# Optimization experiments

Measured on AMD Instinct MI355X. Metric: run time of the kernel, lower is better.

Reference implementation:

```python
import jax, jax.numpy as jnp
import numpy as np

NB, D, ED, N, K, DTR = 4, 1024, 2048, 32, 4, 64
B, L = 1, 1024


def setup_inputs():
    key = jax.random.key(0)
    ks = jax.random.split(key, 10)
    g = lambda k, s, sc=0.02: jax.random.normal(k, s, dtype=jnp.float32) * sc
    A_log = jnp.log(jnp.broadcast_to(jnp.arange(1, N + 1, dtype=jnp.float32), (NB, ED, N))) + 0.0
    return {
        "x": g(ks[0], (B, L, D), 1.0),
        "Wi": g(ks[1], (D, D)),
        "bi": jnp.zeros((D,), jnp.float32),
        "ln_g": jnp.ones((NB, D), jnp.float32),
        "ln_b": jnp.zeros((NB, D), jnp.float32),
        "in_w": g(ks[2], (NB, 2 * ED, D)),
        "conv_w": g(ks[3], (NB, ED, 1, K), 0.2),
        "conv_b": jnp.zeros((NB, ED), jnp.float32),
        "xproj_w": g(ks[4], (NB, DTR + 2 * N, ED)),
        "dtproj_w": g(ks[5], (NB, ED, DTR), 0.1),
        "dtproj_b": jnp.full((NB, ED), -4.0, jnp.float32),
        "A_log": A_log,
        "Dp": jnp.ones((NB, ED), jnp.float32),
        "out_w": g(ks[6], (NB, D, ED)),
        "fn_g": jnp.ones((D,), jnp.float32),
        "fn_b": jnp.zeros((D,), jnp.float32),
        "sp_w": g(ks[7], (N, D)),
        "sp_b": jnp.zeros((N,), jnp.float32),
    }


def layernorm(x, g, b, eps=1e-5):
    m = jnp.mean(x, axis=-1, keepdims=True)
    v = jnp.mean(jnp.square(x - m), axis=-1, keepdims=True)
    return (x - m) * jax.lax.rsqrt(v + eps) * g + b


def mamba(u_in, in_w, conv_w, conv_b, xproj_w, dtproj_w, dtproj_b, A_log, Dp, out_w):
    # u_in: (B, L, D)
    xz = u_in @ in_w.T                       # (B, L, 2*ED)
    u, z = jnp.split(xz, 2, axis=-1)         # each (B, L, ED)
    # causal depthwise conv over time
    uc = jnp.swapaxes(u, 1, 2)               # (B, ED, L)
    uc = jax.lax.conv_general_dilated(uc, conv_w, (1,), [(K - 1, 0)], feature_group_count=ED)
    uc = uc + conv_b[None, :, None]
    u = jax.nn.silu(jnp.swapaxes(uc, 1, 2))  # (B, L, ED)
    x_dbl = u @ xproj_w.T                    # (B, L, DTR + 2N)
    dt, Bm, Cm = jnp.split(x_dbl, [DTR, DTR + N], axis=-1)
    delta = jax.nn.softplus(dt @ dtproj_w.T + dtproj_b)  # (B, L, ED)
    A = -jnp.exp(A_log)                                  # (ED, N)
    dA = jnp.exp(delta[..., None] * A)                   # (B, L, ED, N)
    dBu = (delta * u)[..., None] * Bm[:, :, None, :]     # (B, L, ED, N)

    def step(h, inp):
        dA_t, dBu_t, C_t = inp
        h = dA_t * h + dBu_t
        y = jnp.einsum('ben,bn->be', h, C_t)
        return h, y

    h0 = jnp.zeros((u.shape[0], ED, N), u.dtype)
    _, ys = jax.lax.scan(step, h0, (jnp.swapaxes(dA, 0, 1), jnp.swapaxes(dBu, 0, 1), jnp.swapaxes(Cm, 0, 1)))
    y = jnp.swapaxes(ys, 0, 1) + u * Dp      # (B, L, ED)
    y = y * jax.nn.silu(z)
    return y @ out_w.T                       # (B, L, D)


def reference(x, Wi, bi, ln_g, ln_b, in_w, conv_w, conv_b, xproj_w, dtproj_w, dtproj_b, A_log, Dp, out_w, fn_g, fn_b, sp_w, sp_b):
    h = x @ Wi.T + bi
    for i in range(NB):
        normed = layernorm(h, ln_g[i], ln_b[i])
        h = h + mamba(normed, in_w[i], conv_w[i], conv_b[i], xproj_w[i],
                      dtproj_w[i], dtproj_b[i], A_log[i], Dp[i], out_w[i])
    h = layernorm(h, fn_g, fn_b)
    state = jnp.mean(h, axis=1) @ sp_w.T + sp_b   # (B, N)
    return h, state
```

## Files before the change

kernel.cpp:

```cpp
#include <hip/hip_runtime.h>
#include <math.h>

#define D_    1024
#define ED_   2048
#define NST   32
#define KCONV 4
#define DTR_  64
#define L_    1024
#define NB_   4
#define NCH   8
#define CHUNK (L_ / NCH)
#define ZSPL  4
#define XPZ   16

typedef __bf16 bf16_8 __attribute__((ext_vector_type(8)));
typedef __bf16 bf16_4 __attribute__((ext_vector_type(4)));
typedef float  f32x4  __attribute__((ext_vector_type(4)));

__device__ __forceinline__ float softplus_f(float x) {
  return x > 20.f ? x : log1pf(expf(x));
}
__device__ __forceinline__ float silu_f(float x) {
  return x / (1.f + expf(-x));
}

__device__ __forceinline__ int xcd_swz(int lin, int nwg) {
  const int q = nwg >> 3;
  return (lin & 7) * q + (lin >> 3);
}

__global__ __launch_bounds__(256) void f2bf4_k(
    const float* __restrict__ i0, __bf16* __restrict__ o0, int n0,
    const float* __restrict__ i1, __bf16* __restrict__ o1, int n1,
    const float* __restrict__ i2, __bf16* __restrict__ o2, int n2,
    const float* __restrict__ i3, __bf16* __restrict__ o3, int n3)
{
  int gid = blockIdx.x * 256 + threadIdx.x;
  const int u0 = n0 >> 3, u1 = n1 >> 3, u2 = n2 >> 3, u3 = n3 >> 3;
  const float* in; __bf16* out;
  if (gid < u0) { in = i0; out = o0; }
  else if ((gid -= u0) < u1) { in = i1; out = o1; }
  else if ((gid -= u1) < u2) { in = i2; out = o2; }
  else if ((gid -= u2) < u3) { in = i3; out = o3; }
  else return;
  const int i = gid * 8;
  const float4 a = *reinterpret_cast<const float4*>(in + i);
  const float4 b = *reinterpret_cast<const float4*>(in + i + 4);
  bf16_8 v;
  v[0]=(__bf16)a.x; v[1]=(__bf16)a.y; v[2]=(__bf16)a.z; v[3]=(__bf16)a.w;
  v[4]=(__bf16)b.x; v[5]=(__bf16)b.y; v[6]=(__bf16)b.z; v[7]=(__bf16)b.w;
  *reinterpret_cast<bf16_8*>(out + i) = v;
}

__global__ __launch_bounds__(256) void gemm_mfma(
    const __bf16* __restrict__ A, int lda,
    const __bf16* __restrict__ W, int ldw,
    const float* __restrict__ bias, float* __restrict__ C, int ldc,
    int K, int flags)
{
  __shared__ __bf16 As[128 * 64];
  __shared__ __bf16 Ws[128 * 64];
  const int tid  = threadIdx.x;
  const int lane = tid & 63;
  const int w    = tid >> 6;
  const int wr   = w >> 1, wc = w & 1;
  const int nwg  = gridDim.x * gridDim.y;
  const int swz  = xcd_swz(blockIdx.y * gridDim.x + blockIdx.x, nwg);
  const int bx   = swz % gridDim.x, by = swz / gridDim.x;
  const int row0 = by * 128, col0 = bx * 128;

  f32x4 acc[4][4] = {};

  for (int k0 = 0; k0 < K; k0 += 64) {
    #pragma unroll
    for (int j = 0; j < 4; ++j) {
      const int inst = w * 4 + j;
      const int row  = inst * 8 + (lane >> 3);
      const int lu   = (lane & 7) ^ (row & 7);
      __builtin_amdgcn_global_load_lds(
          (const __attribute__((address_space(1))) void*)(A + (size_t)(row0 + row) * lda + k0 + lu * 8),
          (__attribute__((address_space(3))) void*)(&As[inst * 512]), 16, 0, 0);
      __builtin_amdgcn_global_load_lds(
          (const __attribute__((address_space(1))) void*)(W + (size_t)(col0 + row) * ldw + k0 + lu * 8),
          (__attribute__((address_space(3))) void*)(&Ws[inst * 512]), 16, 0, 0);
    }
    __syncthreads();
    const int r16 = lane & 15;
    const int uq  = lane >> 4;
    #pragma unroll
    for (int ks = 0; ks < 2; ++ks) {
      bf16_8 af[4], bfr[4];
      #pragma unroll
      for (int m = 0; m < 4; ++m) {
        const int row = wr * 64 + m * 16 + r16;
        const int pu  = (ks * 4 + uq) ^ (row & 7);
        af[m] = *reinterpret_cast<const bf16_8*>(&As[row * 64 + pu * 8]);
      }
      #pragma unroll
      for (int n = 0; n < 4; ++n) {
        const int row = wc * 64 + n * 16 + r16;
        const int pu  = (ks * 4 + uq) ^ (row & 7);
        bfr[n] = *reinterpret_cast<const bf16_8*>(&Ws[row * 64 + pu * 8]);
      }
      #pragma unroll
      for (int m = 0; m < 4; ++m)
        #pragma unroll
        for (int n = 0; n < 4; ++n)
          acc[m][n] = __builtin_amdgcn_mfma_f32_16x16x32_bf16(af[m], bfr[n], acc[m][n], 0, 0, 0);
    }
    __syncthreads();
  }

  const int crow = (lane >> 4) * 4;
  const int ccol = lane & 15;
  #pragma unroll
  for (int m = 0; m < 4; ++m)
    #pragma unroll
    for (int n = 0; n < 4; ++n) {
      const int col = col0 + wc * 64 + n * 16 + ccol;
      const float bv = (flags & 4) ? bias[col] : 0.f;
      #pragma unroll
      for (int r = 0; r < 4; ++r) {
        const int row = row0 + wr * 64 + m * 16 + crow + r;
        float* cp = C + (size_t)row * ldc + col;
        float v = acc[m][n][r] + bv;
        if (flags & 2) v = softplus_f(v);
        if (flags & 1) v += *cp;
        *cp = v;
      }
    }
}

__global__ __launch_bounds__(256) void gemm_mfma_sk(
    const __bf16* __restrict__ A, const __bf16* __restrict__ W,
    float* __restrict__ partials, int M, int N, int K, int Kc)
{
  __shared__ __bf16 As[128 * 64];
  __shared__ __bf16 Ws[128 * 64];
  const int tid  = threadIdx.x;
  const int lane = tid & 63;
  const int w    = tid >> 6;
  const int wr   = w >> 1, wc = w & 1;
  const int nwg  = gridDim.x * gridDim.y * gridDim.z;
  const int lin  = (blockIdx.z * gridDim.y + blockIdx.y) * gridDim.x + blockIdx.x;
  const int swz  = xcd_swz(lin, nwg);
  const int bx   = swz % gridDim.x;
  const int tmp  = swz / gridDim.x;
  const int by   = tmp % gridDim.y, bz = tmp / gridDim.y;
  const int row0 = by * 128, col0 = bx * 128;
  const int kbase = bz * Kc;

  f32x4 acc[4][4] = {};

  for (int k0 = kbase; k0 < kbase + Kc; k0 += 64) {
    #pragma unroll
    for (int j = 0; j < 4; ++j) {
      const int inst = w * 4 + j;
      const int row  = inst * 8 + (lane >> 3);
      const int lu   = (lane & 7) ^ (row & 7);
      __builtin_amdgcn_global_load_lds(
          (const __attribute__((address_space(1))) void*)(A + (size_t)(row0 + row) * K + k0 + lu * 8),
          (__attribute__((address_space(3))) void*)(&As[inst * 512]), 16, 0, 0);
      __builtin_amdgcn_global_load_lds(
          (const __attribute__((address_space(1))) void*)(W + (size_t)(col0 + row) * K + k0 + lu * 8),
          (__attribute__((address_space(3))) void*)(&Ws[inst * 512]), 16, 0, 0);
    }
    __syncthreads();
    const int r16 = lane & 15;
    const int uq  = lane >> 4;
    #pragma unroll
    for (int ks = 0; ks < 2; ++ks) {
      bf16_8 af[4], bfr[4];
      #pragma unroll
      for (int m = 0; m < 4; ++m) {
        const int row = wr * 64 + m * 16 + r16;
        const int pu  = (ks * 4 + uq) ^ (row & 7);
        af[m] = *reinterpret_cast<const bf16_8*>(&As[row * 64 + pu * 8]);
      }
      #pragma unroll
      for (int n = 0; n < 4; ++n) {
        const int row = wc * 64 + n * 16 + r16;
        const int pu  = (ks * 4 + uq) ^ (row & 7);
        bfr[n] = *reinterpret_cast<const bf16_8*>(&Ws[row * 64 + pu * 8]);
      }
      #pragma unroll
      for (int m = 0; m < 4; ++m)
        #pragma unroll
        for (int n = 0; n < 4; ++n)
          acc[m][n] = __builtin_amdgcn_mfma_f32_16x16x32_bf16(af[m], bfr[n], acc[m][n], 0, 0, 0);
    }
    __syncthreads();
  }

  float* base = partials + (size_t)bz * M * N;
  const int crow = (lane >> 4) * 4;
  const int ccol = lane & 15;
  #pragma unroll
  for (int m = 0; m < 4; ++m)
    #pragma unroll
    for (int n = 0; n < 4; ++n) {
      const int col = col0 + wc * 64 + n * 16 + ccol;
      #pragma unroll
      for (int r = 0; r < 4; ++r) {
        const int row = row0 + wr * 64 + m * 16 + crow + r;
        base[(size_t)row * N + col] = acc[m][n][r];
      }
    }
}

__global__ __launch_bounds__(256) void mfma_sk_reduce(
    const float* __restrict__ partials, const float* __restrict__ bias,
    float* __restrict__ C, __bf16* __restrict__ Cbf,
    int elems, int ncols, int nz, int flags)
{
  const int i = (blockIdx.x * 256 + threadIdx.x) * 4;
  if (i >= elems) return;
  float4 s = *reinterpret_cast<const float4*>(partials + i);
  for (int z = 1; z < nz; ++z) {
    const float4 p = *reinterpret_cast<const float4*>(partials + (size_t)z * elems + i);
    s.x += p.x; s.y += p.y; s.z += p.z; s.w += p.w;
  }
  if (flags & 4) {
    const float4 bv = *reinterpret_cast<const float4*>(bias + (i % ncols));
    s.x += bv.x; s.y += bv.y; s.z += bv.z; s.w += bv.w;
  }
  if (flags & 1) {
    const float4 ov = *reinterpret_cast<const float4*>(C + i);
    s.x += ov.x; s.y += ov.y; s.z += ov.z; s.w += ov.w;
  }
  *reinterpret_cast<float4*>(C + i) = s;
  if (flags & 8) {
    bf16_4 b;
    b[0]=(__bf16)s.x; b[1]=(__bf16)s.y; b[2]=(__bf16)s.z; b[3]=(__bf16)s.w;
    *reinterpret_cast<bf16_4*>(Cbf + i) = b;
  }
}

__global__ __launch_bounds__(256) void layernorm_k(
    const float* __restrict__ x, const float* __restrict__ g,
    const float* __restrict__ b, float* __restrict__ out)
{
  __shared__ float red[8];
  const int row = blockIdx.x;
  const int tid = threadIdx.x;
  const float* xr = x + (size_t)row * D_;
  float4 v = *reinterpret_cast<const float4*>(xr + tid * 4);
  float s = v.x + v.y + v.z + v.w;
  #pragma unroll
  for (int off = 32; off; off >>= 1) s += __shfl_down(s, off, 64);
  if ((tid & 63) == 0) red[tid >> 6] = s;
  __syncthreads();
  const float m = (red[0] + red[1] + red[2] + red[3]) * (1.f / D_);
  float dx0 = v.x - m, dx1 = v.y - m, dx2 = v.z - m, dx3 = v.w - m;
  float ss = dx0*dx0 + dx1*dx1 + dx2*dx2 + dx3*dx3;
  #pragma unroll
  for (int off = 32; off; off >>= 1) ss += __shfl_down(ss, off, 64);
  if ((tid & 63) == 0) red[4 + (tid >> 6)] = ss;
  __syncthreads();
  const float var = (red[4] + red[5] + red[6] + red[7]) * (1.f / D_);
  const float rs = rsqrtf(var + 1e-5f);
  const int c = tid * 4;
  const float4 gv = *reinterpret_cast<const float4*>(g + c);
  const float4 bv = *reinterpret_cast<const float4*>(b + c);
  float4 o;
  o.x = dx0 * rs * gv.x + bv.x;
  o.y = dx1 * rs * gv.y + bv.y;
  o.z = dx2 * rs * gv.z + bv.z;
  o.w = dx3 * rs * gv.w + bv.w;
  *reinterpret_cast<float4*>(out + (size_t)row * D_ + c) = o;
}

__global__ __launch_bounds__(256) void layernorm_bf_k(
    const float* __restrict__ x, const float* __restrict__ g,
    const float* __restrict__ b, __bf16* __restrict__ out)
{
  __shared__ float red[8];
  const int row = blockIdx.x;
  const int tid = threadIdx.x;
  const float* xr = x + (size_t)row * D_;
  float4 v = *reinterpret_cast<const float4*>(xr + tid * 4);
  float s = v.x + v.y + v.z + v.w;
  #pragma unroll
  for (int off = 32; off; off >>= 1) s += __shfl_down(s, off, 64);
  if ((tid & 63) == 0) red[tid >> 6] = s;
  __syncthreads();
  const float m = (red[0] + red[1] + red[2] + red[3]) * (1.f / D_);
  float dx0 = v.x - m, dx1 = v.y - m, dx2 = v.z - m, dx3 = v.w - m;
  float ss = dx0*dx0 + dx1*dx1 + dx2*dx2 + dx3*dx3;
  #pragma unroll
  for (int off = 32; off; off >>= 1) ss += __shfl_down(ss, off, 64);
  if ((tid & 63) == 0) red[4 + (tid >> 6)] = ss;
  __syncthreads();
  const float var = (red[4] + red[5] + red[6] + red[7]) * (1.f / D_);
  const float rs = rsqrtf(var + 1e-5f);
  const int c = tid * 4;
  const float4 gv = *reinterpret_cast<const float4*>(g + c);
  const float4 bv = *reinterpret_cast<const float4*>(b + c);
  bf16_4 o;
  o[0] = (__bf16)(dx0 * rs * gv.x + bv.x);
  o[1] = (__bf16)(dx1 * rs * gv.y + bv.y);
  o[2] = (__bf16)(dx2 * rs * gv.z + bv.z);
  o[3] = (__bf16)(dx3 * rs * gv.w + bv.w);
  *reinterpret_cast<bf16_4*>(out + (size_t)row * D_ + c) = o;
}

__global__ __launch_bounds__(256) void conv_silu_k(
    const float* __restrict__ xz, const float* __restrict__ cw,
    const float* __restrict__ cb, float* __restrict__ u, __bf16* __restrict__ ub)
{
  const int e = blockIdx.x * 256 + threadIdx.x;
  const int t0 = blockIdx.y * 8;
  const float w0 = cw[e*4+0], w1 = cw[e*4+1], w2 = cw[e*4+2], w3 = cw[e*4+3];
  const float b = cb[e];
  float x0 = (t0 >= 3) ? xz[(size_t)(t0-3)*(2*ED_)+e] : 0.f;
  float x1 = (t0 >= 2) ? xz[(size_t)(t0-2)*(2*ED_)+e] : 0.f;
  float x2 = (t0 >= 1) ? xz[(size_t)(t0-1)*(2*ED_)+e] : 0.f;
  #pragma unroll
  for (int j = 0; j < 8; ++j) {
    const float x3 = xz[(size_t)(t0+j)*(2*ED_)+e];
    const float uv = silu_f(b + w0*x0 + w1*x1 + w2*x2 + w3*x3);
    u[(size_t)(t0+j)*ED_+e] = uv;
    ub[(size_t)(t0+j)*ED_+e] = (__bf16)uv;
    x0 = x1; x1 = x2; x2 = x3;
  }
}

__global__ __launch_bounds__(512) void scan_phase1(
    const float* __restrict__ delta, const float* __restrict__ u,
    const float* __restrict__ xdbl, const float* __restrict__ A_log,
    float* __restrict__ hend, float* __restrict__ Pend)
{
  __shared__ float dl[16][16], ul[16][16];
  __shared__ float bl[16][36];
  const int tid = threadIdx.x;
  const int n = tid & 31;
  const int c = tid >> 5;
  const int e0 = blockIdx.x * 16;
  const int e = e0 + c;
  const int ch = blockIdx.y;
  const float a = -expf(A_log[e * NST + n]);
  float h = 0.f, S = 0.f;
  const int t0 = ch * CHUNK;
  const int s_t = (tid & 255) >> 4, s_e = tid & 15;
  const int bidx = tid - 256;
  const int b_t = bidx >> 3, b_c = (bidx & 7) * 4;

  float rg_a = 0.f;
  float4 rg_b;
  if (tid < 256) {
    rg_a = delta[(size_t)(t0 + s_t) * ED_ + e0 + s_e];
  } else {
    rg_a = u[(size_t)(t0 + s_t) * ED_ + e0 + s_e];
    if (bidx < 128)
      rg_b = *reinterpret_cast<const float4*>(&xdbl[(size_t)(t0 + b_t) * 128 + 64 + b_c]);
  }

  for (int tb = 0; tb < CHUNK; tb += 16) {
    if (tid < 256) {
      dl[s_t][s_e] = rg_a;
    } else {
      ul[s_t][s_e] = rg_a;
      if (bidx < 128) *reinterpret_cast<float4*>(&bl[b_t][b_c]) = rg_b;
    }
    __syncthreads();
    if (tb + 16 < CHUNK) {
      const int t = t0 + tb + 16 + s_t;
      if (tid < 256) {
        rg_a = delta[(size_t)t * ED_ + e0 + s_e];
      } else {
        rg_a = u[(size_t)t * ED_ + e0 + s_e];
        if (bidx < 128)
          rg_b = *reinterpret_cast<const float4*>(&xdbl[(size_t)(t0 + tb + 16 + b_t) * 128 + 64 + b_c]);
      }
    }
    #pragma unroll
    for (int j = 0; j < 16; ++j) {
      const float sd = dl[j][c];
      const float uv = ul[j][c];
      const float Bv = bl[j][n];
      h = fmaf(__expf(sd * a), h, sd * uv * Bv);
      S += sd;
    }
    __syncthreads();
  }
  const int idx = ch * (ED_ * NST) + blockIdx.x * 512 + tid;
  hend[idx] = h;
  Pend[idx] = __expf(a * S);
}

__global__ __launch_bounds__(512) void scan_phase3(
    const float* __restrict__ delta, const float* __restrict__ u,
    const float* __restrict__ xdbl, const float* __restrict__ A_log,
    const float* __restrict__ hend, const float* __restrict__ Pend,
    const float* __restrict__ Dp,
    const float* __restrict__ xz, __bf16* __restrict__ y)
{
  __shared__ float p_lds[16][16][33];
  __shared__ float dl[16][16], ul[16][16], zl[16][16];
  __shared__ float bc[16][68];
  const int tid = threadIdx.x;
  const int n = tid & 31;
  const int c = tid >> 5;
  const int e0 = blockIdx.x * 16;
  const int e = e0 + c;
  const int ch = blockIdx.y;
  const float a = -expf(A_log[e * NST + n]);
  const float dp = Dp[e];

  float h = 0.f;
  {
    const int sidx = blockIdx.x * 512 + tid;
    for (int cc = 0; cc < ch; ++cc) {
      const int off = cc * (ED_ * NST) + sidx;
      h = fmaf(Pend[off], h, hend[off]);
    }
  }

  const int t0 = ch * CHUNK;
  const int r = n & 15, half = n >> 4;
  const int s_t  = (tid & 255) >> 4;
  const int s_e  = tid & 15;
  const int bidx = tid - 256;
  const int b_t  = (bidx & 255) >> 4;
  const int b_c  = (bidx & 15) * 4;

  float rg_a = 0.f, rg_z = 0.f;
  float4 rg_bc;
  {
    const int t = t0 + s_t;
    if (tid < 256) {
      rg_a = delta[(size_t)t * ED_ + e0 + s_e];
      rg_z = xz[(size_t)t * (2*ED_) + ED_ + e0 + s_e];
    } else {
      rg_a = u[(size_t)t * ED_ + e0 + s_e];
      rg_bc = *reinterpret_cast<const float4*>(&xdbl[(size_t)(t0 + b_t) * 128 + 64 + b_c]);
    }
  }

  for (int tb = 0; tb < CHUNK; tb += 16) {
    if (tid < 256) {
      dl[s_t][s_e] = rg_a; zl[s_t][s_e] = rg_z;
    } else {
      ul[s_t][s_e] = rg_a;
      *reinterpret_cast<float4*>(&bc[b_t][b_c]) = rg_bc;
    }
    __syncthreads();
    if (tb + 16 < CHUNK) {
      const int t = t0 + tb + 16 + s_t;
      if (tid < 256) {
        rg_a = delta[(size_t)t * ED_ + e0 + s_e];
        rg_z = xz[(size_t)t * (2*ED_) + ED_ + e0 + s_e];
      } else {
        rg_a = u[(size_t)t * ED_ + e0 + s_e];
        rg_bc = *reinterpret_cast<const float4*>(&xdbl[(size_t)(t0 + tb + 16 + b_t) * 128 + 64 + b_c]);
      }
    }
    #pragma unroll
    for (int j = 0; j < 16; ++j) {
      const float sd = dl[j][c];
      const float uv = ul[j][c];
      const float Bv = bc[j][n];
      const float Cv = bc[j][32 + n];
      const float dA = __expf(sd * a);
      h = fmaf(dA, h, sd * uv * Bv);
      p_lds[c][j][n] = h * Cv;
    }
    __syncthreads();
    float s = 0.f;
    #pragma unroll
    for (int k = 0; k < 16; ++k) s += p_lds[c][r][half * 16 + k];
    s += __shfl_xor(s, 16, 64);
    if (half == 0) {
      const float uvt = ul[r][c];
      const float zv  = zl[r][c];
      y[(size_t)(t0 + tb + r) * ED_ + e] = (__bf16)((s + uvt * dp) * silu_f(zv));
    }
    __syncthreads();
  }
}

__global__ __launch_bounds__(256) void colmean_part_k(
    const float* __restrict__ hf, float* __restrict__ part)
{
  const int d = blockIdx.x * 256 + threadIdx.x;
  const int tc = blockIdx.y;
  float s = 0.f;
  #pragma unroll 8
  for (int j = 0; j < 32; ++j) s += hf[(size_t)(tc * 32 + j) * D_ + d];
  part[tc * D_ + d] = s;
}

__global__ __launch_bounds__(256) void state_fused_k(
    const float* __restrict__ part, const float* __restrict__ spw,
    const float* __restrict__ spb, float* __restrict__ out)
{
  __shared__ float red[4];
  const int nidx = blockIdx.x;
  const int tid = threadIdx.x;
  float s = 0.f;
  for (int d = tid; d < D_; d += 256) {
    float cm = 0.f;
    #pragma unroll
    for (int c = 0; c < 32; ++c) cm += part[c * D_ + d];
    s += cm * (1.f / L_) * spw[(size_t)nidx * D_ + d];
  }
  #pragma unroll
  for (int off = 32; off; off >>= 1) s += __shfl_down(s, off, 64);
  if ((tid & 63) == 0) red[tid >> 6] = s;
  __syncthreads();
  if (tid == 0) out[nidx] = red[0] + red[1] + red[2] + red[3] + spb[nidx];
}

extern "C" void kernel_launch(void* const* d_in, const int* in_sizes, int n_in,
                              void* d_out, int out_size, void* d_ws, size_t ws_size,
                              hipStream_t stream) {
  const float* x        = (const float*)d_in[0];
  const float* Wi       = (const float*)d_in[1];
  const float* bi       = (const float*)d_in[2];
  const float* ln_g     = (const float*)d_in[3];
  const float* ln_b     = (const float*)d_in[4];
  const float* in_w     = (const float*)d_in[5];
  const float* conv_w   = (const float*)d_in[6];
  const float* conv_b   = (const float*)d_in[7];
  const float* xproj_w  = (const float*)d_in[8];
  const float* dtproj_w = (const float*)d_in[9];
  const float* dtproj_b = (const float*)d_in[10];
  const float* A_log    = (const float*)d_in[11];
  const float* Dp       = (const float*)d_in[12];
  const float* out_w    = (const float*)d_in[13];
  const float* fn_g     = (const float*)d_in[14];
  const float* fn_b     = (const float*)d_in[15];
  const float* sp_w     = (const float*)d_in[16];
  const float* sp_b     = (const float*)d_in[17];
  float* out  = (float*)d_out;
  float* ws_f = (float*)d_ws;

  float* h_buf  = ws_f;
  float* xz     = ws_f + 1048576;
  float* u_buf  = ws_f + 5242880;
  float* xdbl   = ws_f + 7340032;
  float* delta  = ws_f + 7471104;
  float* hend   = ws_f + 9568256;
  float* pend   = ws_f + 10092544;
  __bf16* nbf   = (__bf16*)(ws_f + 10617856);
  __bf16* ybf   = (__bf16*)(ws_f + 11142144);
  __bf16* wbf   = (__bf16*)(ws_f + 12190720);
  __bf16* xdblbf= (__bf16*)(ws_f + 16385024);
  __bf16* dtwbf = (__bf16*)(ws_f + 16450560);
  __bf16* ubf   = (__bf16*)(ws_f + 16516096);
  __bf16* xpbf  = (__bf16*)(ws_f + 17564672);
  __bf16* owbf  = (__bf16*)(ws_f + 17695744);
  float* skmf   = u_buf;
  float* skxp   = delta;
  float* cmpart = hend;

  const dim3 blk(256);
  const dim3 blk512(512);

  f2bf4_k<<<1024, blk, 0, stream>>>(x, nbf, L_*D_, Wi, wbf, D_*D_,
                                    x, nbf, 0, x, nbf, 0);
  gemm_mfma_sk<<<dim3(D_/128, L_/128, ZSPL), blk, 0, stream>>>(
      nbf, wbf, skmf, L_, D_, D_, D_/ZSPL);
  mfma_sk_reduce<<<dim3(L_*D_/4/256), blk, 0, stream>>>(
      skmf, bi, h_buf, nullptr, L_*D_, D_, ZSPL, 4);

  for (int i = 0; i < NB_; ++i) {
    f2bf4_k<<<3264, blk, 0, stream>>>(
        in_w    + (size_t)i*2*ED_*D_, wbf,   2*ED_*D_,
        xproj_w + (size_t)i*128*ED_,  xpbf,  128*ED_,
        dtproj_w+ (size_t)i*ED_*DTR_, dtwbf, ED_*DTR_,
        out_w   + (size_t)i*D_*ED_,   owbf,  D_*ED_);
    layernorm_bf_k<<<L_, blk, 0, stream>>>(h_buf, ln_g + i*D_, ln_b + i*D_, nbf);
    gemm_mfma<<<dim3(2*ED_/128, L_/128), blk, 0, stream>>>(
        nbf, D_, wbf, D_, nullptr, xz, 2*ED_, D_, 0);
    conv_silu_k<<<dim3(ED_/256, L_/8), blk, 0, stream>>>(
        xz, conv_w + (size_t)i*ED_*KCONV, conv_b + (size_t)i*ED_, u_buf, ubf);
    gemm_mfma_sk<<<dim3(1, L_/128, XPZ), blk, 0, stream>>>(
        ubf, xpbf, skxp, L_, 128, ED_, ED_/XPZ);
    mfma_sk_reduce<<<dim3(L_*128/4/256), blk, 0, stream>>>(
        skxp, nullptr, xdbl, xdblbf, L_*128, 128, XPZ, 8);
    gemm_mfma<<<dim3(ED_/128, L_/128), blk, 0, stream>>>(
        xdblbf, 128, dtwbf, DTR_, dtproj_b + (size_t)i*ED_, delta, ED_, DTR_, 2 | 4);
    scan_phase1<<<dim3(ED_/16, NCH), blk512, 0, stream>>>(
        delta, u_buf, xdbl, A_log + (size_t)i*ED_*NST, hend, pend);
    scan_phase3<<<dim3(ED_/16, NCH), blk512, 0, stream>>>(
        delta, u_buf, xdbl, A_log + (size_t)i*ED_*NST, hend, pend,
        Dp + (size_t)i*ED_, xz, ybf);
    gemm_mfma_sk<<<dim3(D_/128, L_/128, ZSPL), blk, 0, stream>>>(
        ybf, owbf, skmf, L_, D_, ED_, ED_/ZSPL);
    mfma_sk_reduce<<<dim3(L_*D_/4/256), blk, 0, stream>>>(
        skmf, nullptr, h_buf, nullptr, L_*D_, D_, ZSPL, 1);
  }

  layernorm_k<<<L_, blk, 0, stream>>>(h_buf, fn_g, fn_b, out);
  colmean_part_k<<<dim3(D_/256, 32), blk, 0, stream>>>(out, cmpart);
  state_fused_k<<<NST, blk, 0, stream>>>(cmpart, sp_w, sp_b, out + (size_t)L_*D_);
}
```

Measured before the change: 661.5 us.

## Fuse split-K reduce with next layernorm and pair scan steps

Replaces the split-K reduction plus the separate bf16 layernorm with one kernel that reduces partials, adds the residual, writes h, and emits the next block's normalized bf16 input. This removes one launch and one full re-read of h per block. The scan kernels now combine two recurrence steps per iteration to shorten the serial dependency chain. Phase1 loads 32 timesteps per tile using all threads. Phase3 stores per-state partial products in bf16 shared memory to cut LDS footprint, at some cost in precision.

```diff
diff --git a/kernel.cpp b/kernel.cpp
--- a/kernel.cpp
+++ b/kernel.cpp
@@ -236,6 +236,56 @@
   }
 }
 
+__global__ __launch_bounds__(256) void reduce_ln_k(
+    const float* __restrict__ partials, const float* __restrict__ bias,
+    float* __restrict__ hbuf, const float* __restrict__ g,
+    const float* __restrict__ b, __bf16* __restrict__ outbf, int flags)
+{
+  __shared__ float red[8];
+  const int row = blockIdx.x;
+  const int tid = threadIdx.x;
+  const int c = tid * 4;
+  const size_t off = (size_t)row * D_ + c;
+  float4 v = *reinterpret_cast<const float4*>(partials + off);
+  #pragma unroll
+  for (int z = 1; z < ZSPL; ++z) {
+    const float4 p = *reinterpret_cast<const float4*>(partials + (size_t)z * (L_*D_) + off);
+    v.x += p.x; v.y += p.y; v.z += p.z; v.w += p.w;
+  }
+  if (flags & 4) {
+    const float4 bv = *reinterpret_cast<const float4*>(bias + c);
+    v.x += bv.x; v.y += bv.y; v.z += bv.z; v.w += bv.w;
+  }
+  if (flags & 1) {
+    const float4 ov = *reinterpret_cast<const float4*>(hbuf + off);
+    v.x += ov.x; v.y += ov.y; v.z += ov.z; v.w += ov.w;
+  }
+  *reinterpret_cast<float4*>(hbuf + off) = v;
+
+  float s = v.x + v.y + v.z + v.w;
+  #pragma unroll
+  for (int o = 32; o; o >>= 1) s += __shfl_down(s, o, 64);
+  if ((tid & 63) == 0) red[tid >> 6] = s;
+  __syncthreads();
+  const float m = (red[0] + red[1] + red[2] + red[3]) * (1.f / D_);
+  float dx0 = v.x - m, dx1 = v.y - m, dx2 = v.z - m, dx3 = v.w - m;
+  float ss = dx0*dx0 + dx1*dx1 + dx2*dx2 + dx3*dx3;
+  #pragma unroll
+  for (int o = 32; o; o >>= 1) ss += __shfl_down(ss, o, 64);
+  if ((tid & 63) == 0) red[4 + (tid >> 6)] = ss;
+  __syncthreads();
+  const float var = (red[4] + red[5] + red[6] + red[7]) * (1.f / D_);
+  const float rs = rsqrtf(var + 1e-5f);
+  const float4 gv = *reinterpret_cast<const float4*>(g + c);
+  const float4 bv = *reinterpret_cast<const float4*>(b + c);
+  bf16_4 o;
+  o[0] = (__bf16)(dx0 * rs * gv.x + bv.x);
+  o[1] = (__bf16)(dx1 * rs * gv.y + bv.y);
+  o[2] = (__bf16)(dx2 * rs * gv.z + bv.z);
+  o[3] = (__bf16)(dx3 * rs * gv.w + bv.w);
+  *reinterpret_cast<bf16_4*>(outbf + off) = o;
+}
+
 __global__ __launch_bounds__(256) void layernorm_k(
     const float* __restrict__ x, const float* __restrict__ g,
     const float* __restrict__ b, float* __restrict__ out)
@@ -270,40 +320,6 @@
   *reinterpret_cast<float4*>(out + (size_t)row * D_ + c) = o;
 }
 
-__global__ __launch_bounds__(256) void layernorm_bf_k(
-    const float* __restrict__ x, const float* __restrict__ g,
-    const float* __restrict__ b, __bf16* __restrict__ out)
-{
-  __shared__ float red[8];
-  const int row = blockIdx.x;
-  const int tid = threadIdx.x;
-  const float* xr = x + (size_t)row * D_;
-  float4 v = *reinterpret_cast<const float4*>(xr + tid * 4);
-  float s = v.x + v.y + v.z + v.w;
-  #pragma unroll
-  for (int off = 32; off; off >>= 1) s += __shfl_down(s, off, 64);
-  if ((tid & 63) == 0) red[tid >> 6] = s;
-  __syncthreads();
-  const float m = (red[0] + red[1] + red[2] + red[3]) * (1.f / D_);
-  float dx0 = v.x - m, dx1 = v.y - m, dx2 = v.z - m, dx3 = v.w - m;
-  float ss = dx0*dx0 + dx1*dx1 + dx2*dx2 + dx3*dx3;
-  #pragma unroll
-  for (int off = 32; off; off >>= 1) ss += __shfl_down(ss, off, 64);
-  if ((tid & 63) == 0) red[4 + (tid >> 6)] = ss;
-  __syncthreads();
-  const float var = (red[4] + red[5] + red[6] + red[7]) * (1.f / D_);
-  const float rs = rsqrtf(var + 1e-5f);
-  const int c = tid * 4;
-  const float4 gv = *reinterpret_cast<const float4*>(g + c);
-  const float4 bv = *reinterpret_cast<const float4*>(b + c);
-  bf16_4 o;
-  o[0] = (__bf16)(dx0 * rs * gv.x + bv.x);
-  o[1] = (__bf16)(dx1 * rs * gv.y + bv.y);
-  o[2] = (__bf16)(dx2 * rs * gv.z + bv.z);
-  o[3] = (__bf16)(dx3 * rs * gv.w + bv.w);
-  *reinterpret_cast<bf16_4*>(out + (size_t)row * D_ + c) = o;
-}
-
 __global__ __launch_bounds__(256) void conv_silu_k(
     const float* __restrict__ xz, const float* __restrict__ cw,
     const float* __restrict__ cb, float* __restrict__ u, __bf16* __restrict__ ub)
@@ -330,8 +346,8 @@
     const float* __restrict__ xdbl, const float* __restrict__ A_log,
     float* __restrict__ hend, float* __restrict__ Pend)
 {
-  __shared__ float dl[16][16], ul[16][16];
-  __shared__ float bl[16][36];
+  __shared__ float dl[32][16], ul[32][16];
+  __shared__ float bl[32][36];
   const int tid = threadIdx.x;
   const int n = tid & 31;
   const int c = tid >> 5;
@@ -341,45 +357,38 @@
   const float a = -expf(A_log[e * NST + n]);
   float h = 0.f, S = 0.f;
   const int t0 = ch * CHUNK;
-  const int s_t = (tid & 255) >> 4, s_e = tid & 15;
-  const int bidx = tid - 256;
-  const int b_t = bidx >> 3, b_c = (bidx & 7) * 4;
-
-  float rg_a = 0.f;
+  const int s_t = tid >> 4, s_e = tid & 15;
+  const int b_t = tid >> 3, b_c = (tid & 7) * 4;
+
+  float rg_d, rg_u;
   float4 rg_b;
-  if (tid < 256) {
-    rg_a = delta[(size_t)(t0 + s_t) * ED_ + e0 + s_e];
-  } else {
-    rg_a = u[(size_t)(t0 + s_t) * ED_ + e0 + s_e];
-    if (bidx < 128)
-      rg_b = *reinterpret_cast<const float4*>(&xdbl[(size_t)(t0 + b_t) * 128 + 64 + b_c]);
-  }
-
-  for (int tb = 0; tb < CHUNK; tb += 16) {
-    if (tid < 256) {
-      dl[s_t][s_e] = rg_a;
-    } else {
-      ul[s_t][s_e] = rg_a;
-      if (bidx < 128) *reinterpret_cast<float4*>(&bl[b_t][b_c]) = rg_b;
-    }
-    __syncthreads();
-    if (tb + 16 < CHUNK) {
-      const int t = t0 + tb + 16 + s_t;
-      if (tid < 256) {
-        rg_a = delta[(size_t)t * ED_ + e0 + s_e];
-      } else {
-        rg_a = u[(size_t)t * ED_ + e0 + s_e];
-        if (bidx < 128)
-          rg_b = *reinterpret_cast<const float4*>(&xdbl[(size_t)(t0 + tb + 16 + b_t) * 128 + 64 + b_c]);
-      }
-    }
-    #pragma unroll
-    for (int j = 0; j < 16; ++j) {
-      const float sd = dl[j][c];
-      const float uv = ul[j][c];
-      const float Bv = bl[j][n];
-      h = fmaf(__expf(sd * a), h, sd * uv * Bv);
-      S += sd;
+  rg_d = delta[(size_t)(t0 + s_t) * ED_ + e0 + s_e];
+  rg_u = u[(size_t)(t0 + s_t) * ED_ + e0 + s_e];
+  if (tid < 256)
+    rg_b = *reinterpret_cast<const float4*>(&xdbl[(size_t)(t0 + b_t) * 128 + 64 + b_c]);
+
+  for (int tb = 0; tb < CHUNK; tb += 32) {
+    dl[s_t][s_e] = rg_d;
+    ul[s_t][s_e] = rg_u;
+    if (tid < 256) *reinterpret_cast<float4*>(&bl[b_t][b_c]) = rg_b;
+    __syncthreads();
+    if (tb + 32 < CHUNK) {
+      const int t = t0 + tb + 32 + s_t;
+      rg_d = delta[(size_t)t * ED_ + e0 + s_e];
+      rg_u = u[(size_t)t * ED_ + e0 + s_e];
+      if (tid < 256)
+        rg_b = *reinterpret_cast<const float4*>(&xdbl[(size_t)(t0 + tb + 32 + b_t) * 128 + 64 + b_c]);
+    }
+    #pragma unroll
+    for (int jp = 0; jp < 16; ++jp) {
+      const float sd1 = dl[2*jp][c],   uv1 = ul[2*jp][c],   B1 = bl[2*jp][n];
+      const float sd2 = dl[2*jp+1][c], uv2 = ul[2*jp+1][c], B2 = bl[2*jp+1][n];
+      const float dA1 = __expf(sd1 * a);
+      const float dA2 = __expf(sd2 * a);
+      const float b1 = sd1 * uv1 * B1;
+      const float b2 = sd2 * uv2 * B2;
+      h = fmaf(dA1 * dA2, h, fmaf(dA2, b1, b2));
+      S += sd1 + sd2;
     }
     __syncthreads();
   }
@@ -395,7 +404,7 @@
     const float* __restrict__ Dp,
     const float* __restrict__ xz, __bf16* __restrict__ y)
 {
-  __shared__ float p_lds[16][16][33];
+  __shared__ __bf16 p_lds[16][16][34];
   __shared__ float dl[16][16], ul[16][16], zl[16][16];
   __shared__ float bc[16][68];
   const int tid = threadIdx.x;
@@ -456,19 +465,27 @@
       }
     }
     #pragma unroll
-    for (int j = 0; j < 16; ++j) {
-      const float sd = dl[j][c];
-      const float uv = ul[j][c];
-      const float Bv = bc[j][n];
-      const float Cv = bc[j][32 + n];
-      const float dA = __expf(sd * a);
-      h = fmaf(dA, h, sd * uv * Bv);
-      p_lds[c][j][n] = h * Cv;
+    for (int jp = 0; jp < 8; ++jp) {
+      const float sd1 = dl[2*jp][c],   uv1 = ul[2*jp][c];
+      const float sd2 = dl[2*jp+1][c], uv2 = ul[2*jp+1][c];
+      const float B1 = bc[2*jp][n],   C1 = bc[2*jp][32 + n];
+      const float B2 = bc[2*jp+1][n], C2 = bc[2*jp+1][32 + n];
+      const float dA1 = __expf(sd1 * a);
+      const float dA2 = __expf(sd2 * a);
+      const float b1 = sd1 * uv1 * B1;
+      const float b2 = sd2 * uv2 * B2;
+      const float h1 = fmaf(dA1, h, b1);
+      p_lds[c][2*jp][n] = (__bf16)(h1 * C1);
+      h = fmaf(dA1 * dA2, h, fmaf(dA2, b1, b2));
+      p_lds[c][2*jp+1][n] = (__bf16)(h * C2);
     }
     __syncthreads();
     float s = 0.f;
     #pragma unroll
-    for (int k = 0; k < 16; ++k) s += p_lds[c][r][half * 16 + k];
+    for (int k = 0; k < 8; ++k) {
+      const unsigned v = *reinterpret_cast<const unsigned*>(&p_lds[c][r][half * 16 + 2 * k]);
+      s += __uint_as_float(v << 16) + __uint_as_float(v & 0xffff0000u);
+    }
     s += __shfl_xor(s, 16, 64);
     if (half == 0) {
       const float uvt = ul[r][c];
@@ -561,8 +578,8 @@
                                     x, nbf, 0, x, nbf, 0);
   gemm_mfma_sk<<<dim3(D_/128, L_/128, ZSPL), blk, 0, stream>>>(
       nbf, wbf, skmf, L_, D_, D_, D_/ZSPL);
-  mfma_sk_reduce<<<dim3(L_*D_/4/256), blk, 0, stream>>>(
-      skmf, bi, h_buf, nullptr, L_*D_, D_, ZSPL, 4);
+  reduce_ln_k<<<L_, blk, 0, stream>>>(
+      skmf, bi, h_buf, ln_g, ln_b, nbf, 4);
 
   for (int i = 0; i < NB_; ++i) {
     f2bf4_k<<<3264, blk, 0, stream>>>(
@@ -570,7 +587,6 @@
         xproj_w + (size_t)i*128*ED_,  xpbf,  128*ED_,
         dtproj_w+ (size_t)i*ED_*DTR_, dtwbf, ED_*DTR_,
         out_w   + (size_t)i*D_*ED_,   owbf,  D_*ED_);
-    layernorm_bf_k<<<L_, blk, 0, stream>>>(h_buf, ln_g + i*D_, ln_b + i*D_, nbf);
     gemm_mfma<<<dim3(2*ED_/128, L_/128), blk, 0, stream>>>(
         nbf, D_, wbf, D_, nullptr, xz, 2*ED_, D_, 0);
     conv_silu_k<<<dim3(ED_/256, L_/8), blk, 0, stream>>>(
@@ -588,8 +604,13 @@
         Dp + (size_t)i*ED_, xz, ybf);
     gemm_mfma_sk<<<dim3(D_/128, L_/128, ZSPL), blk, 0, stream>>>(
         ybf, owbf, skmf, L_, D_, ED_, ED_/ZSPL);
-    mfma_sk_reduce<<<dim3(L_*D_/4/256), blk, 0, stream>>>(
-        skmf, nullptr, h_buf, nullptr, L_*D_, D_, ZSPL, 1);
+    if (i < NB_ - 1) {
+      reduce_ln_k<<<L_, blk, 0, stream>>>(
+          skmf, nullptr, h_buf, ln_g + (i+1)*D_, ln_b + (i+1)*D_, nbf, 1);
+    } else {
+      mfma_sk_reduce<<<dim3(L_*D_/4/256), blk, 0, stream>>>(
+          skmf, nullptr, h_buf, nullptr, L_*D_, D_, ZSPL, 1);
+    }
   }
 
   layernorm_k<<<L_, blk, 0, stream>>>(h_buf, fn_g, fn_b, out);
```

Result: no change. 656.8 us (-0.7%).
